# Optimization experiments

Hardware: AMD Instinct MI355X
Metric: run time of the kernel (lower is better)

The kernel has to match this reference:

```python
import jax, jax.numpy as jnp
import numpy as np


def setup_inputs() -> dict:
    key = jax.random.key(0)
    k1, k2, k3 = jax.random.split(key, 3)
    backbone_feature = jax.random.normal(k1, (8, 256), dtype=jnp.float32)
    grouping_result = jax.random.randint(k2, (8,), 0, 32, dtype=jnp.int64)
    feature = jax.random.normal(k3, (8, 32, 48, 48, 48), dtype=jnp.float32)
    return {"backbone_feature": backbone_feature,
            "grouping_result": grouping_result,
            "feature": feature}


def reference(backbone_feature, grouping_result, feature):
    # feature: [B, R, W, H, D]
    B, R, W, H, D = feature.shape
    dt = feature.dtype
    mgr = feature.mean()  # global mean over all samples/regions/voxels

    # --- per-region argmax position (first occurrence, matching strict '>' scan) ---
    flat = feature.reshape(B, R, W * H * D)
    am = jnp.argmax(flat, axis=-1)                      # [B, R]
    max_x = (am // (H * D)).astype(dt)                  # [B, R]
    max_y = ((am // D) % H).astype(dt)
    max_z = (am % D).astype(dt)

    i = jnp.arange(W, dtype=dt).reshape(1, 1, W, 1, 1)
    j = jnp.arange(H, dtype=dt).reshape(1, 1, 1, H, 1)
    k = jnp.arange(D, dtype=dt).reshape(1, 1, 1, 1, D)

    dx2 = (max_x[:, :, None, None, None] - i) ** 2      # [B,R,W,1,1]
    dy2 = (max_y[:, :, None, None, None] - j) ** 2      # [B,R,1,H,1]
    dz2 = (max_z[:, :, None, None, None] - k) ** 2      # [B,R,1,1,D]

    f2 = feature * feature
    # NOTE: faithful to original parenthesization: z-term is NOT weighted by region^2
    dis_loss = jnp.sum(f2 * (dx2 + dy2)) + jnp.sum(jnp.broadcast_to(dz2, (B, R, W, H, D)))

    # --- exclude-self max over regions via top-2 along region axis ---
    srt = jnp.sort(feature, axis=1)                     # ascending along R
    m1 = srt[:, -1]                                     # [B, W, H, D] max over regions
    m2 = srt[:, -2]                                     # second max
    argmax_r = jnp.argmax(feature, axis=1)              # [B, W, H, D] first-occurrence
    r_ids = jnp.arange(R).reshape(1, R, 1, 1, 1)
    max_others = jnp.where(r_ids == argmax_r[:, None], m2[:, None], m1[:, None])  # [B,R,W,H,D]

    div_loss = jnp.sum(f2 * (max_others - mgr) ** 2)

    sum_num = B * R * W * H * D
    return (jnp.reshape(dis_loss / sum_num, (1,)),
            jnp.reshape(div_loss / sum_num, (1,)))
```

## Files before the change

### kernel.cpp

```cpp
#include <hip/hip_runtime.h>
#include <math.h>

#define W48 48
#define HD 2304
#define WHD 110592
#define NR 32
#define NB 8
#define QPP 27648
#define CHUNKS 108
#define MAIN_BLOCKS 864
#define NTOT 28311552.0

struct PPart { float s0, sx, sy; unsigned key; unsigned idx; };

__global__ __launch_bounds__(256, 4)
void k_main(const float* __restrict__ feat, PPart* __restrict__ pp,
            double* __restrict__ blk) {
  __shared__ float    lds_s0[16 * 256];
  __shared__ unsigned lds_key[16 * 256];
  __shared__ unsigned lds_mc[256];
  __shared__ float comb_s0[256], comb_sx[256], comb_sy[256];
  __shared__ unsigned comb_key[256], comb_idx[256];
  __shared__ double ld[4][5];

  const int bid = blockIdx.x;
  const int t = threadIdx.x;
  const int b = bid / CHUNKS;
  const int chunk = bid - b * CHUNKS;
  const int qbase = chunk * 256 + t;
  const float4* gptr = reinterpret_cast<const float4*>(feat) + (size_t)b * (NR * QPP) + qbase;

  const int p0 = qbase * 4;
  const float fi = (float)(p0 / HD);
  const float fj = (float)((p0 / W48) % W48);
  const float rrq = fi * fi + fj * fj;

  float v1[4], v2[4], cp[4];
#pragma unroll
  for (int c = 0; c < 4; ++c) { v1[c] = -INFINITY; v2[c] = -INFINITY; cp[c] = 0.f; }
  float ssum = 0.f, sii = 0.f;
  unsigned mcpack = 0u;

  float4 nb0 = gptr[0];
  float4 nb1 = gptr[QPP];
  float4 nb2 = gptr[2 * (size_t)QPP];

  for (int half = 0; half < 2; ++half) {
#pragma unroll 4
    for (int rr = 0; rr < 16; ++rr) {
      const int r = half * 16 + rr;
      float4 v = nb0; nb0 = nb1; nb1 = nb2;
      if (r < NR - 3) nb2 = gptr[(size_t)(r + 3) * QPP];

      float vv[4] = {v.x, v.y, v.z, v.w};
      float f2[4];
#pragma unroll
      for (int c = 0; c < 4; ++c) {
        float f = vv[c];
        f2[c] = f * f;
        cp[c] += f2[c];
        ssum += f;
        float nv2 = fmaxf(f, v2[c]);
        v2[c] = (f > v1[c]) ? v1[c] : nv2;
        v1[c] = fmaxf(v1[c], f);
      }
      float s0t = (f2[0] + f2[1]) + (f2[2] + f2[3]);
      sii += s0t * rrq;

      float mv = vv[0]; int mc = 0;
#pragma unroll
      for (int c = 1; c < 4; ++c) { if (vv[c] > mv) { mv = vv[c]; mc = c; } }
      unsigned u = __float_as_uint(mv);
      unsigned key = u ^ ((unsigned)((int)u >> 31) | 0x80000000u);

      mcpack |= (unsigned)mc << (2 * rr);
      lds_s0[rr * 256 + t] = s0t;
      lds_key[rr * 256 + t] = key;
    }

    lds_mc[t] = mcpack; mcpack = 0u;
    __syncthreads();
    const int er = t & 15;
    const int eg = t >> 4;
    float es0 = 0.f, esx = 0.f, esy = 0.f;
    unsigned bk = 0u; int brow = 0;
#pragma unroll
    for (int k = 0; k < 16; ++k) {
      int row = eg * 16 + ((k + er) & 15);
      float s0v   = lds_s0[er * 256 + row];
      unsigned kv = lds_key[er * 256 + row];
      unsigned q = (unsigned)(chunk * 256 + row);
      float fiq = (float)(q / 576u);
      float fjq = (float)((q / 12u) % 48u);
      es0 += s0v;
      esx = fmaf(s0v, fiq, esx);
      esy = fmaf(s0v, fjq, esy);
      if (kv > bk || (kv == bk && row < brow)) { bk = kv; brow = row; }
    }
    unsigned wmc = (lds_mc[brow] >> (2 * er)) & 3u;
    unsigned bidx = (unsigned)((chunk * 256 + brow) * 4) + wmc;
    __syncthreads();
    comb_s0[t] = es0; comb_sx[t] = esx; comb_sy[t] = esy;
    comb_key[t] = bk; comb_idx[t] = bidx;
    __syncthreads();
    if (t < 16) {
      float ps0 = 0.f, psx = 0.f, psy = 0.f;
      unsigned fk = 0u, fidx = 0xffffffffu;
#pragma unroll
      for (int g2 = 0; g2 < 16; ++g2) {
        int ii = g2 * 16 + t;
        ps0 += comb_s0[ii]; psx += comb_sx[ii]; psy += comb_sy[ii];
        unsigned ck = comb_key[ii], ci = comb_idx[ii];
        if (ck > fk || (ck == fk && ci < fidx)) { fk = ck; fidx = ci; }
      }
      int plane = b * NR + half * 16 + t;
      PPart o; o.s0 = ps0; o.sx = psx; o.sy = psy; o.key = fk; o.idx = fidx;
      pp[(size_t)plane * CHUNKS + chunk] = o;
    }
  }

  float A = 0.f, Bs = 0.f, C = 0.f;
#pragma unroll
  for (int c = 0; c < 4; ++c) {
    float m1 = v1[c], m1sq = m1 * m1;
    float rest = cp[c] - m1sq;
    A  += m1sq * rest + v2[c] * v2[c] * m1sq;
    Bs += m1 * rest + v2[c] * m1sq;
    C  += cp[c];
  }
  double dA = A, dB = Bs, dC = C, dS = ssum, dI = sii;
  const int wave = t >> 6, lane = t & 63;
#pragma unroll
  for (int off = 32; off; off >>= 1) {
    dA += __shfl_down(dA, off);
    dB += __shfl_down(dB, off);
    dC += __shfl_down(dC, off);
    dS += __shfl_down(dS, off);
    dI += __shfl_down(dI, off);
  }
  if (lane == 0) { ld[wave][0]=dA; ld[wave][1]=dB; ld[wave][2]=dC; ld[wave][3]=dS; ld[wave][4]=dI; }
  __syncthreads();
  if (t == 0) {
    double a=0, bb=0, cc=0, ss=0, si=0;
#pragma unroll
    for (int w = 0; w < 4; ++w) { a+=ld[w][0]; bb+=ld[w][1]; cc+=ld[w][2]; ss+=ld[w][3]; si+=ld[w][4]; }
    blk[(size_t)bid*5+0]=a; blk[(size_t)bid*5+1]=bb; blk[(size_t)bid*5+2]=cc;
    blk[(size_t)bid*5+3]=ss; blk[(size_t)bid*5+4]=si;
  }
}

__global__ __launch_bounds__(128)
void k_planes(const PPart* __restrict__ pp, double* __restrict__ planeDis) {
  const int p = blockIdx.x;
  const int t = threadIdx.x;
  double s0 = 0, sx = 0, sy = 0;
  unsigned fkey = 0, idx = 0xffffffffu;
  if (t < CHUNKS) {
    PPart v = pp[(size_t)p * CHUNKS + t];
    s0 = v.s0; sx = v.sx; sy = v.sy; fkey = v.key; idx = v.idx;
  }
#pragma unroll
  for (int off = 32; off; off >>= 1) {
    s0 += __shfl_down(s0, off);
    sx += __shfl_down(sx, off);
    sy += __shfl_down(sy, off);
    unsigned ok = __shfl_down(fkey, off);
    unsigned oi = __shfl_down(idx, off);
    if (ok > fkey || (ok == fkey && oi < idx)) { fkey = ok; idx = oi; }
  }
  __shared__ double ls[2][3];
  __shared__ unsigned lk[2][2];
  const int wave = t >> 6, lane = t & 63;
  if (lane == 0) { ls[wave][0]=s0; ls[wave][1]=sx; ls[wave][2]=sy; lk[wave][0]=fkey; lk[wave][1]=idx; }
  __syncthreads();
  if (t == 0) {
    double a0=0, a1=0, a2=0; unsigned bk=0, bi=0xffffffffu;
#pragma unroll
    for (int w = 0; w < 2; ++w) {
      a0 += ls[w][0]; a1 += ls[w][1]; a2 += ls[w][2];
      if (lk[w][0] > bk || (lk[w][0]==bk && lk[w][1] < bi)) { bk = lk[w][0]; bi = lk[w][1]; }
    }
    int am = (int)bi;
    int mx = am / HD;
    int rem = am - mx * HD;
    int my = rem / W48;
    int mz = rem - my * W48;
    double dmx = mx, dmy = my, dmz = mz;
    planeDis[p] = (dmx*dmx + dmy*dmy) * a0 - 2.0*dmx*a1 - 2.0*dmy*a2
                + 2304.0 * (48.0*dmz*dmz - 2256.0*dmz + 35720.0);
  }
}

__global__ __launch_bounds__(256)
void k_fin(const double* __restrict__ planeDis, const double* __restrict__ blk,
           float* __restrict__ out) {
  const int t = threadIdx.x;
  double dis = planeDis[t];
  double A = 0, B = 0, C = 0, S = 0, SII = 0;
  for (int i = t; i < MAIN_BLOCKS; i += 256) {
    A   += blk[(size_t)i*5+0];
    B   += blk[(size_t)i*5+1];
    C   += blk[(size_t)i*5+2];
    S   += blk[(size_t)i*5+3];
    SII += blk[(size_t)i*5+4];
  }
#pragma unroll
  for (int off = 32; off; off >>= 1) {
    dis += __shfl_down(dis, off);
    A   += __shfl_down(A, off);
    B   += __shfl_down(B, off);
    C   += __shfl_down(C, off);
    S   += __shfl_down(S, off);
    SII += __shfl_down(SII, off);
  }
  __shared__ double ls[4][6];
  const int wave = t >> 6, lane = t & 63;
  if (lane == 0) {
    ls[wave][0]=dis; ls[wave][1]=A; ls[wave][2]=B; ls[wave][3]=C; ls[wave][4]=S; ls[wave][5]=SII;
  }
  __syncthreads();
  if (t == 0) {
    double td=0, tA=0, tB=0, tC=0, tS=0, tI=0;
#pragma unroll
    for (int w = 0; w < 4; ++w) {
      td+=ls[w][0]; tA+=ls[w][1]; tB+=ls[w][2]; tC+=ls[w][3]; tS+=ls[w][4]; tI+=ls[w][5];
    }
    double mgr = tS / NTOT;
    out[0] = (float)((td + tI) / NTOT);
    out[1] = (float)((tA - 2.0*mgr*tB + mgr*mgr*tC) / NTOT);
  }
}

extern "C" void kernel_launch(void* const* d_in, const int* in_sizes, int n_in,
                              void* d_out, int out_size, void* d_ws, size_t ws_size,
                              hipStream_t stream) {
  const float* feat = (const float*)d_in[2];
  float* out = (float*)d_out;

  PPart* pp = (PPart*)d_ws;
  double* blk = (double*)((char*)d_ws + 552960);
  double* planeDis = (double*)((char*)d_ws + 552960 + 34560);

  k_main<<<MAIN_BLOCKS, 256, 0, stream>>>(feat, pp, blk);
  k_planes<<<256, 128, 0, stream>>>(pp, planeDis);
  k_fin<<<1, 256, 0, stream>>>(planeDis, blk, out);
}
```

Baseline: 39.15 us.

## Use 64-thread main blocks and merge plane/final reductions with last-block atomic

Main kernel shrinks blocks to a single 64-lane wave (4x more blocks), replacing LDS cross-wave combining with xor shuffles and deepening the register prefetch to four regions. The argmax key encoding is replaced by float max comparisons and precomputed LDS coordinates. The plane and final reduction kernels are merged into one kernel that uses an atomic counter so the last block computes the outputs, removing a launch but adding a memset and a workspace counter. The aim is to cut block-level sync and launch overhead and raise memory-level parallelism, at the cost of more partial records to reduce.

New measurement: 60.28 us. +54.0%, slower.

```diff
diff --git a/kernel.cpp b/kernel.cpp
--- a/kernel.cpp
+++ b/kernel.cpp
@@ -7,33 +7,39 @@
 #define NR 32
 #define NB 8
 #define QPP 27648
-#define CHUNKS 108
-#define MAIN_BLOCKS 864
+#define TPB 64
+#define CHUNKS 432
+#define MAIN_BLOCKS 3456
 #define NTOT 28311552.0
 
-struct PPart { float s0, sx, sy; unsigned key; unsigned idx; };
-
-__global__ __launch_bounds__(256, 4)
+struct PPart { float s0, sx, sy, mv; unsigned idx; };
+
+#define PP_OFF   0u
+#define BLK_OFF  2211840u
+#define PD_OFF   2350080u
+#define DP_OFF   2352128u
+#define CNT_OFF  2362368u
+
+__global__ __launch_bounds__(64, 4)
 void k_main(const float* __restrict__ feat, PPart* __restrict__ pp,
             double* __restrict__ blk) {
-  __shared__ float    lds_s0[16 * 256];
-  __shared__ unsigned lds_key[16 * 256];
-  __shared__ unsigned lds_mc[256];
-  __shared__ float comb_s0[256], comb_sx[256], comb_sy[256];
-  __shared__ unsigned comb_key[256], comb_idx[256];
-  __shared__ double ld[4][5];
+  __shared__ float lds_s0[16 * 64];
+  __shared__ float lds_mv[16 * 64];
+  __shared__ float lds_fi[64], lds_fj[64];
+  __shared__ unsigned lds_mc[64];
 
   const int bid = blockIdx.x;
   const int t = threadIdx.x;
   const int b = bid / CHUNKS;
   const int chunk = bid - b * CHUNKS;
-  const int qbase = chunk * 256 + t;
+  const int qbase = chunk * 64 + t;
   const float4* gptr = reinterpret_cast<const float4*>(feat) + (size_t)b * (NR * QPP) + qbase;
 
   const int p0 = qbase * 4;
   const float fi = (float)(p0 / HD);
   const float fj = (float)((p0 / W48) % W48);
   const float rrq = fi * fi + fj * fj;
+  lds_fi[t] = fi; lds_fj[t] = fj;
 
   float v1[4], v2[4], cp[4];
 #pragma unroll
@@ -42,15 +48,17 @@
   unsigned mcpack = 0u;
 
   float4 nb0 = gptr[0];
-  float4 nb1 = gptr[QPP];
+  float4 nb1 = gptr[(size_t)QPP];
   float4 nb2 = gptr[2 * (size_t)QPP];
+  float4 nb3 = gptr[3 * (size_t)QPP];
 
   for (int half = 0; half < 2; ++half) {
 #pragma unroll 4
     for (int rr = 0; rr < 16; ++rr) {
       const int r = half * 16 + rr;
-      float4 v = nb0; nb0 = nb1; nb1 = nb2;
-      if (r < NR - 3) nb2 = gptr[(size_t)(r + 3) * QPP];
+      float4 v = nb0; nb0 = nb1; nb1 = nb2; nb2 = nb3;
+      int rn = r + 4; rn = (rn < NR) ? rn : (NR - 1);
+      nb3 = gptr[(size_t)rn * QPP];
 
       float vv[4] = {v.x, v.y, v.z, v.w};
       float f2[4];
@@ -59,23 +67,19 @@
         float f = vv[c];
         f2[c] = f * f;
         cp[c] += f2[c];
-        ssum += f;
         float nv2 = fmaxf(f, v2[c]);
         v2[c] = (f > v1[c]) ? v1[c] : nv2;
         v1[c] = fmaxf(v1[c], f);
       }
+      ssum += (vv[0] + vv[1]) + (vv[2] + vv[3]);
       float s0t = (f2[0] + f2[1]) + (f2[2] + f2[3]);
       sii += s0t * rrq;
 
-      float mv = vv[0]; int mc = 0;
-#pragma unroll
-      for (int c = 1; c < 4; ++c) { if (vv[c] > mv) { mv = vv[c]; mc = c; } }
-      unsigned u = __float_as_uint(mv);
-      unsigned key = u ^ ((unsigned)((int)u >> 31) | 0x80000000u);
-
+      float mv = fmaxf(fmaxf(vv[0], vv[1]), fmaxf(vv[2], vv[3]));
+      int mc = (mv == vv[0]) ? 0 : ((mv == vv[1]) ? 1 : ((mv == vv[2]) ? 2 : 3));
       mcpack |= (unsigned)mc << (2 * rr);
-      lds_s0[rr * 256 + t] = s0t;
-      lds_key[rr * 256 + t] = key;
+      lds_s0[rr * 64 + t] = s0t;
+      lds_mv[rr * 64 + t] = mv;
     }
 
     lds_mc[t] = mcpack; mcpack = 0u;
@@ -83,40 +87,34 @@
     const int er = t & 15;
     const int eg = t >> 4;
     float es0 = 0.f, esx = 0.f, esy = 0.f;
-    unsigned bk = 0u; int brow = 0;
+    float bmv = -INFINITY; int brow = 0;
 #pragma unroll
     for (int k = 0; k < 16; ++k) {
       int row = eg * 16 + ((k + er) & 15);
-      float s0v   = lds_s0[er * 256 + row];
-      unsigned kv = lds_key[er * 256 + row];
-      unsigned q = (unsigned)(chunk * 256 + row);
-      float fiq = (float)(q / 576u);
-      float fjq = (float)((q / 12u) % 48u);
+      float s0v = lds_s0[er * 64 + row];
+      float mvv = lds_mv[er * 64 + row];
       es0 += s0v;
-      esx = fmaf(s0v, fiq, esx);
-      esy = fmaf(s0v, fjq, esy);
-      if (kv > bk || (kv == bk && row < brow)) { bk = kv; brow = row; }
-    }
-    unsigned wmc = (lds_mc[brow] >> (2 * er)) & 3u;
-    unsigned bidx = (unsigned)((chunk * 256 + brow) * 4) + wmc;
+      esx = fmaf(s0v, lds_fi[row], esx);
+      esy = fmaf(s0v, lds_fj[row], esy);
+      if (mvv > bmv || (mvv == bmv && row < brow)) { bmv = mvv; brow = row; }
+    }
+    unsigned bidx = (unsigned)((chunk * 64 + brow) * 4) + ((lds_mc[brow] >> (2 * er)) & 3u);
+
+#pragma unroll
+    for (int m = 16; m <= 32; m <<= 1) {
+      es0 += __shfl_xor(es0, m);
+      esx += __shfl_xor(esx, m);
+      esy += __shfl_xor(esy, m);
+      float omv = __shfl_xor(bmv, m);
+      unsigned oix = (unsigned)__shfl_xor((int)bidx, m);
+      if (omv > bmv || (omv == bmv && oix < bidx)) { bmv = omv; bidx = oix; }
+    }
+    if (t < 16) {
+      int plane = b * NR + half * 16 + er;
+      PPart o; o.s0 = es0; o.sx = esx; o.sy = esy; o.mv = bmv; o.idx = bidx;
+      pp[(size_t)plane * CHUNKS + chunk] = o;
+    }
     __syncthreads();
-    comb_s0[t] = es0; comb_sx[t] = esx; comb_sy[t] = esy;
-    comb_key[t] = bk; comb_idx[t] = bidx;
-    __syncthreads();
-    if (t < 16) {
-      float ps0 = 0.f, psx = 0.f, psy = 0.f;
-      unsigned fk = 0u, fidx = 0xffffffffu;
-#pragma unroll
-      for (int g2 = 0; g2 < 16; ++g2) {
-        int ii = g2 * 16 + t;
-        ps0 += comb_s0[ii]; psx += comb_sx[ii]; psy += comb_sy[ii];
-        unsigned ck = comb_key[ii], ci = comb_idx[ii];
-        if (ck > fk || (ck == fk && ci < fidx)) { fk = ck; fidx = ci; }
-      }
-      int plane = b * NR + half * 16 + t;
-      PPart o; o.s0 = ps0; o.sx = psx; o.sy = psy; o.key = fk; o.idx = fidx;
-      pp[(size_t)plane * CHUNKS + chunk] = o;
-    }
   }
 
   float A = 0.f, Bs = 0.f, C = 0.f;
@@ -129,7 +127,6 @@
     C  += cp[c];
   }
   double dA = A, dB = Bs, dC = C, dS = ssum, dI = sii;
-  const int wave = t >> 6, lane = t & 63;
 #pragma unroll
   for (int off = 32; off; off >>= 1) {
     dA += __shfl_down(dA, off);
@@ -138,47 +135,52 @@
     dS += __shfl_down(dS, off);
     dI += __shfl_down(dI, off);
   }
-  if (lane == 0) { ld[wave][0]=dA; ld[wave][1]=dB; ld[wave][2]=dC; ld[wave][3]=dS; ld[wave][4]=dI; }
-  __syncthreads();
-  if (t == 0) {
-    double a=0, bb=0, cc=0, ss=0, si=0;
-#pragma unroll
-    for (int w = 0; w < 4; ++w) { a+=ld[w][0]; bb+=ld[w][1]; cc+=ld[w][2]; ss+=ld[w][3]; si+=ld[w][4]; }
-    blk[(size_t)bid*5+0]=a; blk[(size_t)bid*5+1]=bb; blk[(size_t)bid*5+2]=cc;
-    blk[(size_t)bid*5+3]=ss; blk[(size_t)bid*5+4]=si;
+  if (t == 0) {
+    blk[(size_t)bid * 5 + 0] = dA;
+    blk[(size_t)bid * 5 + 1] = dB;
+    blk[(size_t)bid * 5 + 2] = dC;
+    blk[(size_t)bid * 5 + 3] = dS;
+    blk[(size_t)bid * 5 + 4] = dI;
   }
 }
 
-__global__ __launch_bounds__(128)
-void k_planes(const PPart* __restrict__ pp, double* __restrict__ planeDis) {
+__global__ __launch_bounds__(512)
+void k_reduce(const PPart* __restrict__ pp, const double* __restrict__ blk,
+              double* __restrict__ planeDis, double* __restrict__ divpart,
+              unsigned* __restrict__ counter, float* __restrict__ out) {
+  __shared__ double ls[8][3];
+  __shared__ float lmv8[8];
+  __shared__ unsigned lidx8[8];
+  __shared__ double fin[8][6];
+  __shared__ int lastFlag;
+
   const int p = blockIdx.x;
   const int t = threadIdx.x;
+  const int wave = t >> 6, lane = t & 63;
+
   double s0 = 0, sx = 0, sy = 0;
-  unsigned fkey = 0, idx = 0xffffffffu;
+  float mv = -INFINITY; unsigned idx = 0xffffffffu;
   if (t < CHUNKS) {
     PPart v = pp[(size_t)p * CHUNKS + t];
-    s0 = v.s0; sx = v.sx; sy = v.sy; fkey = v.key; idx = v.idx;
+    s0 = v.s0; sx = v.sx; sy = v.sy; mv = v.mv; idx = v.idx;
   }
 #pragma unroll
   for (int off = 32; off; off >>= 1) {
     s0 += __shfl_down(s0, off);
     sx += __shfl_down(sx, off);
     sy += __shfl_down(sy, off);
-    unsigned ok = __shfl_down(fkey, off);
-    unsigned oi = __shfl_down(idx, off);
-    if (ok > fkey || (ok == fkey && oi < idx)) { fkey = ok; idx = oi; }
-  }
-  __shared__ double ls[2][3];
-  __shared__ unsigned lk[2][2];
-  const int wave = t >> 6, lane = t & 63;
-  if (lane == 0) { ls[wave][0]=s0; ls[wave][1]=sx; ls[wave][2]=sy; lk[wave][0]=fkey; lk[wave][1]=idx; }
+    float omv = __shfl_down(mv, off);
+    unsigned oix = (unsigned)__shfl_down((int)idx, off);
+    if (omv > mv || (omv == mv && oix < idx)) { mv = omv; idx = oix; }
+  }
+  if (lane == 0) { ls[wave][0] = s0; ls[wave][1] = sx; ls[wave][2] = sy; lmv8[wave] = mv; lidx8[wave] = idx; }
   __syncthreads();
   if (t == 0) {
-    double a0=0, a1=0, a2=0; unsigned bk=0, bi=0xffffffffu;
-#pragma unroll
-    for (int w = 0; w < 2; ++w) {
+    double a0 = 0, a1 = 0, a2 = 0; float bm = -INFINITY; unsigned bi = 0xffffffffu;
+#pragma unroll
+    for (int w = 0; w < 8; ++w) {
       a0 += ls[w][0]; a1 += ls[w][1]; a2 += ls[w][2];
-      if (lk[w][0] > bk || (lk[w][0]==bk && lk[w][1] < bi)) { bk = lk[w][0]; bi = lk[w][1]; }
+      if (lmv8[w] > bm || (lmv8[w] == bm && lidx8[w] < bi)) { bm = lmv8[w]; bi = lidx8[w]; }
     }
     int am = (int)bi;
     int mx = am / HD;
@@ -189,45 +191,68 @@
     planeDis[p] = (dmx*dmx + dmy*dmy) * a0 - 2.0*dmx*a1 - 2.0*dmy*a2
                 + 2304.0 * (48.0*dmz*dmz - 2256.0*dmz + 35720.0);
   }
-}
-
-__global__ __launch_bounds__(256)
-void k_fin(const double* __restrict__ planeDis, const double* __restrict__ blk,
-           float* __restrict__ out) {
-  const int t = threadIdx.x;
-  double dis = planeDis[t];
-  double A = 0, B = 0, C = 0, S = 0, SII = 0;
-  for (int i = t; i < MAIN_BLOCKS; i += 256) {
-    A   += blk[(size_t)i*5+0];
-    B   += blk[(size_t)i*5+1];
-    C   += blk[(size_t)i*5+2];
-    S   += blk[(size_t)i*5+3];
-    SII += blk[(size_t)i*5+4];
-  }
-#pragma unroll
-  for (int off = 32; off; off >>= 1) {
-    dis += __shfl_down(dis, off);
-    A   += __shfl_down(A, off);
-    B   += __shfl_down(B, off);
-    C   += __shfl_down(C, off);
-    S   += __shfl_down(S, off);
-    SII += __shfl_down(SII, off);
-  }
-  __shared__ double ls[4][6];
-  const int wave = t >> 6, lane = t & 63;
-  if (lane == 0) {
-    ls[wave][0]=dis; ls[wave][1]=A; ls[wave][2]=B; ls[wave][3]=C; ls[wave][4]=S; ls[wave][5]=SII;
+
+  double A = 0, Bs = 0, C = 0, S = 0, SI = 0;
+  if (t < 16) {
+    int i = p + 256 * t;
+    if (i < MAIN_BLOCKS) {
+      const double* bb = blk + (size_t)i * 5;
+      A = bb[0]; Bs = bb[1]; C = bb[2]; S = bb[3]; SI = bb[4];
+    }
+  }
+#pragma unroll
+  for (int off = 8; off; off >>= 1) {
+    A  += __shfl_down(A, off);
+    Bs += __shfl_down(Bs, off);
+    C  += __shfl_down(C, off);
+    S  += __shfl_down(S, off);
+    SI += __shfl_down(SI, off);
+  }
+  if (t == 0) {
+    double* dp = divpart + (size_t)p * 5;
+    dp[0] = A; dp[1] = Bs; dp[2] = C; dp[3] = S; dp[4] = SI;
   }
   __syncthreads();
-  if (t == 0) {
-    double td=0, tA=0, tB=0, tC=0, tS=0, tI=0;
-#pragma unroll
-    for (int w = 0; w < 4; ++w) {
-      td+=ls[w][0]; tA+=ls[w][1]; tB+=ls[w][2]; tC+=ls[w][3]; tS+=ls[w][4]; tI+=ls[w][5];
-    }
-    double mgr = tS / NTOT;
-    out[0] = (float)((td + tI) / NTOT);
-    out[1] = (float)((tA - 2.0*mgr*tB + mgr*mgr*tC) / NTOT);
+
+  if (t == 0) {
+    __threadfence();
+    unsigned old = atomicAdd(counter, 1u);
+    lastFlag = (old == 255u);
+  }
+  __syncthreads();
+  if (lastFlag) {
+    __threadfence();
+    double dis = 0, fA = 0, fB = 0, fC = 0, fS = 0, fI = 0;
+    if (t < 256) {
+      dis = planeDis[t];
+      const double* dp = divpart + (size_t)t * 5;
+      fA = dp[0]; fB = dp[1]; fC = dp[2]; fS = dp[3]; fI = dp[4];
+    }
+#pragma unroll
+    for (int off = 32; off; off >>= 1) {
+      dis += __shfl_down(dis, off);
+      fA  += __shfl_down(fA, off);
+      fB  += __shfl_down(fB, off);
+      fC  += __shfl_down(fC, off);
+      fS  += __shfl_down(fS, off);
+      fI  += __shfl_down(fI, off);
+    }
+    if (lane == 0) {
+      fin[wave][0] = dis; fin[wave][1] = fA; fin[wave][2] = fB;
+      fin[wave][3] = fC;  fin[wave][4] = fS; fin[wave][5] = fI;
+    }
+    __syncthreads();
+    if (t == 0) {
+      double td = 0, tA = 0, tB = 0, tC = 0, tS = 0, tI = 0;
+#pragma unroll
+      for (int w = 0; w < 8; ++w) {
+        td += fin[w][0]; tA += fin[w][1]; tB += fin[w][2];
+        tC += fin[w][3]; tS += fin[w][4]; tI += fin[w][5];
+      }
+      double mgr = tS / NTOT;
+      out[0] = (float)((td + tI) / NTOT);
+      out[1] = (float)((tA - 2.0*mgr*tB + mgr*mgr*tC) / NTOT);
+    }
   }
 }
 
@@ -237,11 +262,13 @@
   const float* feat = (const float*)d_in[2];
   float* out = (float*)d_out;
 
-  PPart* pp = (PPart*)d_ws;
-  double* blk = (double*)((char*)d_ws + 552960);
-  double* planeDis = (double*)((char*)d_ws + 552960 + 34560);
-
-  k_main<<<MAIN_BLOCKS, 256, 0, stream>>>(feat, pp, blk);
-  k_planes<<<256, 128, 0, stream>>>(pp, planeDis);
-  k_fin<<<1, 256, 0, stream>>>(planeDis, blk, out);
+  PPart* pp        = (PPart*)((char*)d_ws + PP_OFF);
+  double* blk      = (double*)((char*)d_ws + BLK_OFF);
+  double* planeDis = (double*)((char*)d_ws + PD_OFF);
+  double* divpart  = (double*)((char*)d_ws + DP_OFF);
+  unsigned* cnt    = (unsigned*)((char*)d_ws + CNT_OFF);
+
+  hipMemsetAsync(cnt, 0, 4, stream);
+  k_main<<<MAIN_BLOCKS, TPB, 0, stream>>>(feat, pp, blk);
+  k_reduce<<<256, 512, 0, stream>>>(pp, blk, planeDis, divpart, cnt, out);
 }
```
